# Performance work log

Measured on AMD Instinct MI355X. Metric: run time of the kernel, lower is better.

The kernel has to match this reference:

```python
import jax, jax.numpy as jnp
import numpy as np

N_VOXELS = 400000
GRID = 128
KSIZE = 3
GROUPS = 4
C_IN = 64
C_OUT = 64


def _build_rulebook(n, grid, ksize, seed=0):
    """Build submanifold-conv neighbor map on host with numpy.

    Returns coords-free neighbor_idx [n, ksize**3] int32; entry k is the index of
    the active voxel at offset k from voxel i, or -1 if that site is inactive.
    """
    rng = np.random.default_rng(seed)
    lin = rng.choice(grid ** 3, size=n, replace=False).astype(np.int64)
    x = lin // (grid * grid)
    y = (lin // grid) % grid
    z = lin % grid
    order = np.argsort(lin)
    sorted_keys = lin[order]
    r = ksize // 2
    nb = np.full((n, ksize ** 3), -1, dtype=np.int32)
    k = 0
    for dx in range(-r, r + 1):
        for dy in range(-r, r + 1):
            for dz in range(-r, r + 1):
                nx, ny, nz = x + dx, y + dy, z + dz
                inb = (nx >= 0) & (nx < grid) & (ny >= 0) & (ny < grid) & (nz >= 0) & (nz < grid)
                nkey = nx * grid * grid + ny * grid + nz
                pos = np.searchsorted(sorted_keys, nkey)
                pos_c = np.minimum(pos, n - 1)
                found = inb & (sorted_keys[pos_c] == nkey)
                nb[:, k] = np.where(found, order[pos_c], -1).astype(np.int32)
                k += 1
    return nb


def setup_inputs() -> dict:
    key = jax.random.key(0)
    k1, k2, k3 = jax.random.split(key, 3)
    cpg_in = C_IN // GROUPS
    cpg_out = C_OUT // GROUPS
    features = jax.random.normal(k1, (N_VOXELS, C_IN), dtype=jnp.float32)
    # weight[g, k, ci, co] for each group g and kernel offset k
    weight = jax.random.normal(k2, (GROUPS, KSIZE ** 3, cpg_in, cpg_out), dtype=jnp.float32) * (1.0 / np.sqrt(cpg_in * KSIZE ** 3))
    bias = jax.random.normal(k3, (C_OUT,), dtype=jnp.float32) * 0.01
    neighbor_idx = jnp.asarray(_build_rulebook(N_VOXELS, GRID, KSIZE))
    return {"features": features, "weight": weight, "bias": bias, "neighbor_idx": neighbor_idx}


def reference(features, weight, bias, neighbor_idx):
    # Grouped submanifold sparse conv: gather -> grouped matmul -> accumulate,
    # over the fixed set of K^3 kernel offsets (output sites == input sites).
    N = features.shape[0]
    G, K, cin, cout = weight.shape
    feat = features.reshape(N, G, cin)
    mask = neighbor_idx >= 0                      # [N, K]
    idx = jnp.where(mask, neighbor_idx, 0)        # safe gather index
    out = jnp.zeros((N, G, cout), dtype=features.dtype)
    for k in range(K):  # K=27 fixed small loop over kernel offsets
        gath = feat[idx[:, k]] * mask[:, k, None, None].astype(features.dtype)  # [N, G, cin]
        out = out + jnp.einsum('ngc,gcd->ngd', gath, weight[:, k])
    out = out.reshape(N, G * cout) + bias
    return out
```

## Files before the change

### kernel.cpp

```cpp
#include <hip/hip_runtime.h>
#include <hip/hip_fp16.h>

#define NVOX 400000
#define KVOL 27
#define CTOT 64
#define NTILES (NVOX / 16)
#define NPAIR 14
#define TILES_PER_BLOCK 10
#define NBLOCKS (NTILES / TILES_PER_BLOCK)
#define WFRAG_HALVES (4 * NPAIR * 64 * 8)

#define FEATH_OFF 0
#define WFRAG_OFF 51200000

typedef __attribute__((ext_vector_type(8))) _Float16 half8;
typedef __attribute__((ext_vector_type(4))) float float4v;

__global__ void cvt_feat_kernel(const float* __restrict__ f, _Float16* __restrict__ fh) {
    int t = blockIdx.x * blockDim.x + threadIdx.x;
    const int total = NVOX * CTOT / 8;
    if (t >= total) return;
    const float4* fp = (const float4*)f + (size_t)t * 2;
    float4 a = fp[0], b = fp[1];
    union { _Float16 h[8]; uint4 u; } r;
    r.h[0] = (_Float16)a.x; r.h[1] = (_Float16)a.y;
    r.h[2] = (_Float16)a.z; r.h[3] = (_Float16)a.w;
    r.h[4] = (_Float16)b.x; r.h[5] = (_Float16)b.y;
    r.h[6] = (_Float16)b.z; r.h[7] = (_Float16)b.w;
    ((uint4*)fh)[t] = r.u;
}

__global__ void cvt_w_kernel(const float* __restrict__ w, _Float16* __restrict__ wf) {
    int t = blockIdx.x * blockDim.x + threadIdx.x;
    if (t >= WFRAG_HALVES) return;
    int j = t & 7;
    int l = (t >> 3) & 63;
    int gp = t >> 9;
    int p = gp % NPAIR;
    int g = gp / NPAIR;
    int co = l & 15;
    int quad = l >> 4;
    int ko = 2 * p + (quad >> 1);
    int ci = (quad & 1) * 8 + j;
    float val = (ko < KVOL) ? w[((g * KVOL + ko) * 16 + ci) * 16 + co] : 0.f;
    wf[t] = (_Float16)val;
}

__global__ __launch_bounds__(256) void conv_main_kernel(
        const _Float16* __restrict__ fh,
        const uint4*    __restrict__ wfrag,
        const float*    __restrict__ bias,
        const int*      __restrict__ nb,
        float* __restrict__ out) {
    __shared__ int s_nb[16 * 28];
    const int t = threadIdx.x;
    const int lane = t & 63;
    const int g = t >> 6;
    const int v = lane & 15;
    const int quad = lane >> 4;
    const int q2 = quad >> 1;
    const int half = quad & 1;
    const int co = lane & 15;

    uint4 wB[NPAIR];
#pragma unroll
    for (int p = 0; p < NPAIR; ++p)
        wB[p] = wfrag[(g * NPAIR + p) * 64 + lane];

    const _Float16* fbase = fh + g * 16 + half * 8;
    const float breg = bias[g * 16 + co];

    const int tile0 = blockIdx.x * TILES_PER_BLOCK;
    for (int tt = 0; tt < TILES_PER_BLOCK; ++tt) {
        const int tile = tile0 + tt;

        __syncthreads();
        const int* src = nb + (size_t)tile * (16 * KVOL);
        for (int j = t; j < 16 * KVOL; j += 256) {
            int vv = j / KVOL;
            int k = j - vv * KVOL;
            s_nb[vv * 28 + k] = src[j];
        }
        if (t < 16) s_nb[t * 28 + 27] = -1;
        __syncthreads();

        int idx[NPAIR];
#pragma unroll
        for (int p = 0; p < NPAIR; ++p)
            idx[p] = s_nb[v * 28 + 2 * p + q2];

        uint4 a[NPAIR];
#pragma unroll
        for (int p = 0; p < NPAIR; ++p) {
            uint4 z = {0u, 0u, 0u, 0u};
            a[p] = z;
            if (idx[p] >= 0)
                a[p] = *(const uint4*)(fbase + (size_t)idx[p] * CTOT);
        }
        __builtin_amdgcn_sched_barrier(0);

        float4v acc0 = {0.f, 0.f, 0.f, 0.f};
        float4v acc1 = {0.f, 0.f, 0.f, 0.f};
#pragma unroll
        for (int p = 0; p < NPAIR; p += 2) {
            acc0 = __builtin_amdgcn_mfma_f32_16x16x32_f16(
                __builtin_bit_cast(half8, a[p]),
                __builtin_bit_cast(half8, wB[p]), acc0, 0, 0, 0);
            acc1 = __builtin_amdgcn_mfma_f32_16x16x32_f16(
                __builtin_bit_cast(half8, a[p + 1]),
                __builtin_bit_cast(half8, wB[p + 1]), acc1, 0, 0, 0);
        }

        float* ob = out + ((size_t)(tile * 16 + quad * 4)) * CTOT + g * 16 + co;
#pragma unroll
        for (int r = 0; r < 4; ++r)
            ob[(size_t)r * CTOT] = acc0[r] + acc1[r] + breg;
    }
}

extern "C" void kernel_launch(void* const* d_in, const int* in_sizes, int n_in,
                              void* d_out, int out_size, void* d_ws, size_t ws_size,
                              hipStream_t stream) {
    const float* features = (const float*)d_in[0];
    const float* weight   = (const float*)d_in[1];
    const float* bias     = (const float*)d_in[2];
    const int*   nb       = (const int*)d_in[3];
    float* out = (float*)d_out;

    char* ws = (char*)d_ws;
    _Float16* featH = (_Float16*)(ws + FEATH_OFF);
    _Float16* wf    = (_Float16*)(ws + WFRAG_OFF);

    cvt_feat_kernel<<<(NVOX * CTOT / 8 + 255) / 256, 256, 0, stream>>>(features, featH);
    cvt_w_kernel<<<(WFRAG_HALVES + 255) / 256, 256, 0, stream>>>(weight, wf);
    conv_main_kernel<<<NBLOCKS, 256, 0, stream>>>(featH, (const uint4*)wf, bias, nb, out);
}
```

Baseline: 310.9 us.

## Fuse conversion kernels, remap blocks per XCD, use nontemporal loads/stores

Merges the feature and weight fp16 conversion kernels into one launch to save a kernel launch. Adds nontemporal loads on the fp32 features and neighbor indices and nontemporal stores on the output, so streaming data does not pollute cache. Remaps block IDs so that consecutive tiles land on the same XCD, which should improve L2 locality for neighbor gathers. It also drops the padded shared-memory layout and the per-element division in the neighbor copy, and instead sets the 27th-offset padding in registers.

```diff
diff --git a/kernel.cpp b/kernel.cpp
--- a/kernel.cpp
+++ b/kernel.cpp
@@ -6,9 +6,11 @@
 #define CTOT 64
 #define NTILES (NVOX / 16)
 #define NPAIR 14
-#define TILES_PER_BLOCK 10
-#define NBLOCKS (NTILES / TILES_PER_BLOCK)
+#define TPB 10
+#define NBLOCKS (NTILES / TPB)
 #define WFRAG_HALVES (4 * NPAIR * 64 * 8)
+#define FEAT_BLOCKS (NVOX * CTOT / 8 / 256)
+#define W_BLOCKS (WFRAG_HALVES / 256)
 
 #define FEATH_OFF 0
 #define WFRAG_OFF 51200000
@@ -16,34 +18,38 @@
 typedef __attribute__((ext_vector_type(8))) _Float16 half8;
 typedef __attribute__((ext_vector_type(4))) float float4v;
 
-__global__ void cvt_feat_kernel(const float* __restrict__ f, _Float16* __restrict__ fh) {
-    int t = blockIdx.x * blockDim.x + threadIdx.x;
-    const int total = NVOX * CTOT / 8;
-    if (t >= total) return;
-    const float4* fp = (const float4*)f + (size_t)t * 2;
-    float4 a = fp[0], b = fp[1];
-    union { _Float16 h[8]; uint4 u; } r;
-    r.h[0] = (_Float16)a.x; r.h[1] = (_Float16)a.y;
-    r.h[2] = (_Float16)a.z; r.h[3] = (_Float16)a.w;
-    r.h[4] = (_Float16)b.x; r.h[5] = (_Float16)b.y;
-    r.h[6] = (_Float16)b.z; r.h[7] = (_Float16)b.w;
-    ((uint4*)fh)[t] = r.u;
-}
-
-__global__ void cvt_w_kernel(const float* __restrict__ w, _Float16* __restrict__ wf) {
-    int t = blockIdx.x * blockDim.x + threadIdx.x;
-    if (t >= WFRAG_HALVES) return;
-    int j = t & 7;
-    int l = (t >> 3) & 63;
-    int gp = t >> 9;
-    int p = gp % NPAIR;
-    int g = gp / NPAIR;
-    int co = l & 15;
-    int quad = l >> 4;
-    int ko = 2 * p + (quad >> 1);
-    int ci = (quad & 1) * 8 + j;
-    float val = (ko < KVOL) ? w[((g * KVOL + ko) * 16 + ci) * 16 + co] : 0.f;
-    wf[t] = (_Float16)val;
+__global__ void cvt_fused_kernel(const float* __restrict__ f,
+                                 const float* __restrict__ w,
+                                 _Float16* __restrict__ fh,
+                                 _Float16* __restrict__ wf) {
+    const int b = blockIdx.x;
+    if (b < FEAT_BLOCKS) {
+        const int t = b * 256 + threadIdx.x;
+        const float4v* fp = (const float4v*)f + (size_t)t * 2;
+        float4v a = __builtin_nontemporal_load(fp);
+        float4v c = __builtin_nontemporal_load(fp + 1);
+        union { _Float16 h[8]; uint4 u; } r;
+        r.h[0] = (_Float16)a[0]; r.h[1] = (_Float16)a[1];
+        r.h[2] = (_Float16)a[2]; r.h[3] = (_Float16)a[3];
+        r.h[4] = (_Float16)c[0]; r.h[5] = (_Float16)c[1];
+        r.h[6] = (_Float16)c[2]; r.h[7] = (_Float16)c[3];
+        ((uint4*)fh)[t] = r.u;
+    } else {
+        const int t = (b - FEAT_BLOCKS) * 256 + threadIdx.x;
+        if (t < WFRAG_HALVES) {
+            int j = t & 7;
+            int l = (t >> 3) & 63;
+            int gp = t >> 9;
+            int p = gp % NPAIR;
+            int g = gp / NPAIR;
+            int co = l & 15;
+            int quad = l >> 4;
+            int ko = 2 * p + (quad >> 1);
+            int ci = (quad & 1) * 8 + j;
+            float val = (ko < KVOL) ? w[((g * KVOL + ko) * 16 + ci) * 16 + co] : 0.f;
+            wf[t] = (_Float16)val;
+        }
+    }
 }
 
 __global__ __launch_bounds__(256) void conv_main_kernel(
@@ -52,7 +58,7 @@
         const float*    __restrict__ bias,
         const int*      __restrict__ nb,
         float* __restrict__ out) {
-    __shared__ int s_nb[16 * 28];
+    __shared__ int s_nb[16 * KVOL];
     const int t = threadIdx.x;
     const int lane = t & 63;
     const int g = t >> 6;
@@ -61,6 +67,13 @@
     const int q2 = quad >> 1;
     const int half = quad & 1;
     const int co = lane & 15;
+    const int vb = v * KVOL;
+
+    const int q_ = NBLOCKS / 8, r_ = NBLOCKS % 8;
+    const int xcd = blockIdx.x & 7;
+    const int chunk = blockIdx.x >> 3;
+    const int wgid = (xcd < r_ ? xcd * (q_ + 1) : r_ * (q_ + 1) + (xcd - r_) * q_) + chunk;
+    const int tile0 = wgid * TPB;
 
     uint4 wB[NPAIR];
 #pragma unroll
@@ -70,32 +83,28 @@
     const _Float16* fbase = fh + g * 16 + half * 8;
     const float breg = bias[g * 16 + co];
 
-    const int tile0 = blockIdx.x * TILES_PER_BLOCK;
-    for (int tt = 0; tt < TILES_PER_BLOCK; ++tt) {
+    for (int tt = 0; tt < TPB; ++tt) {
         const int tile = tile0 + tt;
 
         __syncthreads();
         const int* src = nb + (size_t)tile * (16 * KVOL);
-        for (int j = t; j < 16 * KVOL; j += 256) {
-            int vv = j / KVOL;
-            int k = j - vv * KVOL;
-            s_nb[vv * 28 + k] = src[j];
-        }
-        if (t < 16) s_nb[t * 28 + 27] = -1;
+        for (int j = t; j < 16 * KVOL; j += 256)
+            s_nb[j] = __builtin_nontemporal_load(src + j);
         __syncthreads();
 
-        int idx[NPAIR];
+        int ix[NPAIR];
 #pragma unroll
-        for (int p = 0; p < NPAIR; ++p)
-            idx[p] = s_nb[v * 28 + 2 * p + q2];
+        for (int p = 0; p < NPAIR - 1; ++p)
+            ix[p] = s_nb[vb + 2 * p + q2];
+        ix[NPAIR - 1] = (q2 == 0) ? s_nb[vb + 26] : -1;
 
         uint4 a[NPAIR];
 #pragma unroll
         for (int p = 0; p < NPAIR; ++p) {
             uint4 z = {0u, 0u, 0u, 0u};
             a[p] = z;
-            if (idx[p] >= 0)
-                a[p] = *(const uint4*)(fbase + (size_t)idx[p] * CTOT);
+            if (ix[p] >= 0)
+                a[p] = *(const uint4*)(fbase + (size_t)ix[p] * CTOT);
         }
         __builtin_amdgcn_sched_barrier(0);
 
@@ -114,7 +123,7 @@
         float* ob = out + ((size_t)(tile * 16 + quad * 4)) * CTOT + g * 16 + co;
 #pragma unroll
         for (int r = 0; r < 4; ++r)
-            ob[(size_t)r * CTOT] = acc0[r] + acc1[r] + breg;
+            __builtin_nontemporal_store(acc0[r] + acc1[r] + breg, ob + (size_t)r * CTOT);
     }
 }
 
@@ -131,7 +140,6 @@
     _Float16* featH = (_Float16*)(ws + FEATH_OFF);
     _Float16* wf    = (_Float16*)(ws + WFRAG_OFF);
 
-    cvt_feat_kernel<<<(NVOX * CTOT / 8 + 255) / 256, 256, 0, stream>>>(features, featH);
-    cvt_w_kernel<<<(WFRAG_HALVES + 255) / 256, 256, 0, stream>>>(weight, wf);
+    cvt_fused_kernel<<<FEAT_BLOCKS + W_BLOCKS, 256, 0, stream>>>(features, weight, featH, wf);
     conv_main_kernel<<<NBLOCKS, 256, 0, stream>>>(featH, (const uint4*)wf, bias, nb, out);
 }
```

Result: faster. 301.0 us (-3.2%).
